# Kernel tuning notes

Measured on AMD Instinct MI355X. Metric: run time of the kernel, lower is better.

## Reference

```python
import jax, jax.numpy as jnp
import numpy as np

WINDOW_SIZE = 11
CHANNEL = 1
SIGMA = 1.5


def _gaussian_window(window_size=WINDOW_SIZE, channel=CHANNEL, sigma=SIGMA):
    x = np.arange(window_size)
    g = np.exp(-((x - window_size // 2) ** 2) / (2.0 * sigma ** 2))
    g = g / g.sum()
    w2d = np.outer(g, g).astype(np.float32)  # [K,K]
    # depthwise conv kernel: [C_out=channel, C_in/groups=1, K, K]
    return jnp.asarray(np.broadcast_to(w2d, (channel, 1, window_size, window_size)))


def _dwconv(x, window):
    pad = WINDOW_SIZE // 2
    return jax.lax.conv_general_dilated(
        x, window,
        window_strides=(1, 1),
        padding=[(pad, pad), (pad, pad)],
        dimension_numbers=('NCHW', 'OIHW', 'NCHW'),
        feature_group_count=CHANNEL)


def _ssim(img1, img2, window):
    C1 = 0.01 ** 2
    C2 = 0.03 ** 2
    mu1 = _dwconv(img1, window)
    mu2 = _dwconv(img2, window)
    mu1_sq = mu1 * mu1
    mu2_sq = mu2 * mu2
    mu1_mu2 = mu1 * mu2
    sigma1_sq = _dwconv(img1 * img1, window) - mu1_sq
    sigma2_sq = _dwconv(img2 * img2, window) - mu2_sq
    sigma12 = _dwconv(img1 * img2, window) - mu1_mu2
    ssim_map = ((2.0 * mu1_mu2 + C1) * (2.0 * sigma12 + C2)) / (
        (mu1_sq + mu2_sq + C1) * (sigma1_sq + sigma2_sq + C2))
    return ssim_map.mean()


def setup_inputs() -> dict:
    key = jax.random.key(0)
    k1, k2 = jax.random.split(key)
    B, C, H, W = 64, 1, 512, 512
    pred = jax.random.uniform(k1, (B, C, H, W), dtype=jnp.float32)
    target = jax.random.uniform(k2, (B, C, H, W), dtype=jnp.float32)
    return {"pred": pred, "target": target}


def reference(pred, target):
    window = _gaussian_window()
    return 1.0 - _ssim(pred[:, :1], target[:, :1], window)
```

## Files before the change

kernel.cpp:

```cpp
#include <hip/hip_runtime.h>

#define BATCH 64
#define HH 512
#define WW 512
#define TH 32
#define KS 11
#define PADK 5
#define NIN (TH + 2 * PADK)
#define LROW (WW + 2 * PADK)
#define NPIX (64.0 * 512.0 * 512.0)

__global__ void __launch_bounds__(512, 2) ssim_main_kernel(
    const float* __restrict__ img1, const float* __restrict__ img2,
    double* __restrict__ accum) {
  constexpr float GA[KS] = {
      0.00102838f, 0.00759884f, 0.03600087f, 0.10936069f, 0.21300553f,
      0.26601172f, 0.21300553f, 0.10936069f, 0.03600087f, 0.00759884f,
      0.00102838f};
  const float C1v = 1e-4f, C2v = 9e-4f;

  const int c  = threadIdx.x;
  const int r0 = blockIdx.x * TH;
  const int b  = blockIdx.y;

  const float* __restrict__ p1 = img1 + (size_t)b * (HH * WW);
  const float* __restrict__ p2 = img2 + (size_t)b * (HH * WW);

  __shared__ float4 s4[2][4][LROW];
  __shared__ float wsum[8];

  if (c < PADK) {
#pragma unroll
    for (int bi = 0; bi < 2; ++bi)
#pragma unroll
      for (int r = 0; r < 4; ++r) {
        s4[bi][r][c]             = make_float4(0.f, 0.f, 0.f, 0.f);
        s4[bi][r][WW + PADK + c] = make_float4(0.f, 0.f, 0.f, 0.f);
      }
  }

#define DECLR(s) float zA##s = 0.f, zB##s = 0.f, zQ##s = 0.f, zP##s = 0.f;
  DECLR(0) DECLR(1) DECLR(2) DECLR(3) DECLR(4) DECLR(5)
  DECLR(6) DECLR(7) DECLR(8) DECLR(9) DECLR(10)

  float pa0, pa1, pa2, pa3, pb0, pb1, pb2, pb3;
  float local = 0.f;

#define LD1(k_, j_)                                                     \
  {                                                                     \
    constexpr int rc_ = 4 * (k_) + (j_);                                \
    pa##j_ = 0.f; pb##j_ = 0.f;                                         \
    if constexpr (rc_ < NIN) {                                          \
      const int rr_ = r0 - PADK + rc_;                                  \
      if ((unsigned)rr_ < HH) {                                         \
        const int off_ = rr_ * WW + c;                                  \
        pa##j_ = p1[off_];                                              \
        pb##j_ = p2[off_];                                              \
      }                                                                 \
    }                                                                   \
  }
#define LOADC(k_) { LD1(k_, 0) LD1(k_, 1) LD1(k_, 2) LD1(k_, 3) }

#define WR1(k_, j_)                                                     \
  {                                                                     \
    constexpr int rc_ = 4 * (k_) + (j_);                                \
    if constexpr (rc_ < NIN)                                            \
      s4[(k_) & 1][j_][PADK + c] = make_float4(                         \
          pa##j_, pb##j_, fmaf(pa##j_, pa##j_, pb##j_ * pb##j_),        \
          pa##j_ * pb##j_);                                             \
  }
#define WRITEC(k_) { WR1(k_, 0) WR1(k_, 1) WR1(k_, 2) WR1(k_, 3) }

#define HBODY(bb_, j_, S)                                               \
  {                                                                     \
    float h1 = 0.f, h2 = 0.f, hq = 0.f, hp = 0.f;                       \
    _Pragma("unroll")                                                   \
    for (int k = 0; k < KS; ++k) {                                      \
      const float4 v = s4[bb_][j_][c + k];                              \
      const float w_ = GA[k];                                           \
      h1 = fmaf(w_, v.x, h1);                                           \
      h2 = fmaf(w_, v.y, h2);                                           \
      hq = fmaf(w_, v.z, hq);                                           \
      hp = fmaf(w_, v.w, hp);                                           \
    }                                                                   \
    zA##S = h1; zB##S = h2; zQ##S = hq; zP##S = hp;                     \
  }

#define VC(P, s0,s1,s2v,s3,s4v,s5,s6v,s7,s8,s9,s10)                     \
  fmaf(GA[10], P##s10, fmaf(GA[9], P##s9, fmaf(GA[8], P##s8,            \
  fmaf(GA[7], P##s7, fmaf(GA[6], P##s6v, fmaf(GA[5], P##s5,             \
  fmaf(GA[4], P##s4v, fmaf(GA[3], P##s3, fmaf(GA[2], P##s2v,            \
  fmaf(GA[1], P##s1, GA[0] * P##s0))))))))))

#define VOUTBODY(s0,s1,s2v,s3,s4v,s5,s6v,s7,s8,s9,s10)                  \
  {                                                                     \
    const float m1 = VC(zA, s0,s1,s2v,s3,s4v,s5,s6v,s7,s8,s9,s10);      \
    const float m2 = VC(zB, s0,s1,s2v,s3,s4v,s5,s6v,s7,s8,s9,s10);      \
    const float mq = VC(zQ, s0,s1,s2v,s3,s4v,s5,s6v,s7,s8,s9,s10);      \
    const float mp = VC(zP, s0,s1,s2v,s3,s4v,s5,s6v,s7,s8,s9,s10);      \
    const float m1s = m1 * m1, m2s = m2 * m2, m12 = m1 * m2;            \
    const float s12 = mp - m12;                                         \
    const float sqq = mq - m1s - m2s;                                   \
    const float num = fmaf(2.f, m12, C1v) * fmaf(2.f, s12, C2v);        \
    const float den = (m1s + m2s + C1v) * (sqq + C2v);                  \
    local = fmaf(num, __builtin_amdgcn_rcpf(den), local);               \
  }

#define ROT0  0,1,2,3,4,5,6,7,8,9,10
#define ROT1  1,2,3,4,5,6,7,8,9,10,0
#define ROT2  2,3,4,5,6,7,8,9,10,0,1
#define ROT3  3,4,5,6,7,8,9,10,0,1,2
#define ROT4  4,5,6,7,8,9,10,0,1,2,3
#define ROT5  5,6,7,8,9,10,0,1,2,3,4
#define ROT6  6,7,8,9,10,0,1,2,3,4,5
#define ROT7  7,8,9,10,0,1,2,3,4,5,6
#define ROT8  8,9,10,0,1,2,3,4,5,6,7
#define ROT9  9,10,0,1,2,3,4,5,6,7,8
#define ROT10 10,0,1,2,3,4,5,6,7,8,9
#define VOUTE(...) VOUTBODY(__VA_ARGS__)

#define ROWH(bb_, j_, S)      { HBODY(bb_, j_, S) }
#define ROWO(bb_, j_, S, R_)  { HBODY(bb_, j_, S) VOUTE(R_) }

  LOADC(0)

  WRITEC(0) __syncthreads(); LOADC(1)
  ROWH(0,0,0) ROWH(0,1,1) ROWH(0,2,2) ROWH(0,3,3)
  WRITEC(1) __syncthreads(); LOADC(2)
  ROWH(1,0,4) ROWH(1,1,5) ROWH(1,2,6) ROWH(1,3,7)
  WRITEC(2) __syncthreads(); LOADC(3)
  ROWH(0,0,8) ROWH(0,1,9)
  ROWO(0,2,10, ROT0) ROWO(0,3,0, ROT1)
  WRITEC(3) __syncthreads(); LOADC(4)
  ROWO(1,0,1, ROT2) ROWO(1,1,2, ROT3) ROWO(1,2,3, ROT4) ROWO(1,3,4, ROT5)
  WRITEC(4) __syncthreads(); LOADC(5)
  ROWO(0,0,5, ROT6) ROWO(0,1,6, ROT7) ROWO(0,2,7, ROT8) ROWO(0,3,8, ROT9)
  WRITEC(5) __syncthreads(); LOADC(6)
  ROWO(1,0,9, ROT10) ROWO(1,1,10, ROT0) ROWO(1,2,0, ROT1) ROWO(1,3,1, ROT2)
  WRITEC(6) __syncthreads(); LOADC(7)
  ROWO(0,0,2, ROT3) ROWO(0,1,3, ROT4) ROWO(0,2,4, ROT5) ROWO(0,3,5, ROT6)
  WRITEC(7) __syncthreads(); LOADC(8)
  ROWO(1,0,6, ROT7) ROWO(1,1,7, ROT8) ROWO(1,2,8, ROT9) ROWO(1,3,9, ROT10)
  WRITEC(8) __syncthreads(); LOADC(9)
  ROWO(0,0,10, ROT0) ROWO(0,1,0, ROT1) ROWO(0,2,1, ROT2) ROWO(0,3,2, ROT3)
  WRITEC(9) __syncthreads(); LOADC(10)
  ROWO(1,0,3, ROT4) ROWO(1,1,4, ROT5) ROWO(1,2,5, ROT6) ROWO(1,3,6, ROT7)
  WRITEC(10) __syncthreads();
  ROWO(0,0,7, ROT8) ROWO(0,1,8, ROT9)

#pragma unroll
  for (int off = 32; off > 0; off >>= 1) local += __shfl_down(local, off, 64);
  const int wave = threadIdx.x >> 6;
  const int lane = threadIdx.x & 63;
  if (lane == 0) wsum[wave] = local;
  __syncthreads();
  if (threadIdx.x == 0) {
    float s = 0.f;
#pragma unroll
    for (int w = 0; w < 8; ++w) s += wsum[w];
    atomicAdd(accum, (double)s);
  }
}

__global__ void ssim_final_kernel(const double* __restrict__ accum,
                                  float* __restrict__ out) {
  out[0] = 1.0f - (float)(accum[0] / NPIX);
}

extern "C" void kernel_launch(void* const* d_in, const int* in_sizes, int n_in,
                              void* d_out, int out_size, void* d_ws, size_t ws_size,
                              hipStream_t stream) {
  const float* img1 = (const float*)d_in[0];
  const float* img2 = (const float*)d_in[1];
  double* accum = (double*)d_ws;
  hipMemsetAsync(accum, 0, sizeof(double), stream);

  dim3 grid(HH / TH, BATCH);
  ssim_main_kernel<<<grid, 512, 0, stream>>>(img1, img2, accum);
  ssim_final_kernel<<<1, 1, 0, stream>>>(accum, (float*)d_out);
}
```

Measured before the change: 180.1 us.

## Store only image pairs in LDS and recompute products in horizontal pass

The shared-memory row buffer now holds float2 (img1, img2) pairs instead of float4 with precomputed squared and cross products, halving LDS footprint and write traffic. The horizontal pass reads aligned float4 chunks covering two pixels at a time, using per-thread parity-shifted weights (12 taps with a zero at one end) so odd and even columns share the same aligned reads. Six 16-byte LDS reads replace eleven per row. The cost is recomputing q and p per tap and extra FMAs on zero-weighted taps.

New measurement: 179.0 us. About the same (-0.6%).

```diff
diff --git a/kernel.cpp b/kernel.cpp
--- a/kernel.cpp
+++ b/kernel.cpp
@@ -7,7 +7,7 @@
 #define KS 11
 #define PADK 5
 #define NIN (TH + 2 * PADK)
-#define LROW (WW + 2 * PADK)
+#define NP2 524
 #define NPIX (64.0 * 512.0 * 512.0)
 
 __global__ void __launch_bounds__(512, 2) ssim_main_kernel(
@@ -26,18 +26,32 @@
   const float* __restrict__ p1 = img1 + (size_t)b * (HH * WW);
   const float* __restrict__ p2 = img2 + (size_t)b * (HH * WW);
 
-  __shared__ float4 s4[2][4][LROW];
+  __shared__ __align__(16) float2 s2[2][4][NP2];
   __shared__ float wsum[8];
 
-  if (c < PADK) {
+  if (c < 12) {
+    const int idx = (c < 6) ? c : (512 + c);
 #pragma unroll
     for (int bi = 0; bi < 2; ++bi)
 #pragma unroll
-      for (int r = 0; r < 4; ++r) {
-        s4[bi][r][c]             = make_float4(0.f, 0.f, 0.f, 0.f);
-        s4[bi][r][WW + PADK + c] = make_float4(0.f, 0.f, 0.f, 0.f);
-      }
-  }
+      for (int r = 0; r < 4; ++r) s2[bi][r][idx] = make_float2(0.f, 0.f);
+  }
+
+  const bool oddc = (c & 1);
+  const float w0  = oddc ? GA[0]  : 0.f;
+  const float w1  = oddc ? GA[1]  : GA[0];
+  const float w2  = oddc ? GA[2]  : GA[1];
+  const float w3  = oddc ? GA[3]  : GA[2];
+  const float w4  = oddc ? GA[4]  : GA[3];
+  const float w5  = oddc ? GA[5]  : GA[4];
+  const float w6  = oddc ? GA[6]  : GA[5];
+  const float w7  = oddc ? GA[7]  : GA[6];
+  const float w8  = oddc ? GA[8]  : GA[7];
+  const float w9  = oddc ? GA[9]  : GA[8];
+  const float w10 = oddc ? GA[10] : GA[9];
+  const float w11 = oddc ? 0.f    : GA[10];
+
+  const int pr0 = (c + 1) >> 1;
 
 #define DECLR(s) float zA##s = 0.f, zB##s = 0.f, zQ##s = 0.f, zP##s = 0.f;
   DECLR(0) DECLR(1) DECLR(2) DECLR(3) DECLR(4) DECLR(5)
@@ -65,24 +79,30 @@
   {                                                                     \
     constexpr int rc_ = 4 * (k_) + (j_);                                \
     if constexpr (rc_ < NIN)                                            \
-      s4[(k_) & 1][j_][PADK + c] = make_float4(                         \
-          pa##j_, pb##j_, fmaf(pa##j_, pa##j_, pb##j_ * pb##j_),        \
-          pa##j_ * pb##j_);                                             \
+      s2[(k_) & 1][j_][c + 6] = make_float2(pa##j_, pb##j_);            \
   }
 #define WRITEC(k_) { WR1(k_, 0) WR1(k_, 1) WR1(k_, 2) WR1(k_, 3) }
 
+#define HPX(aa_, bb2_, w_)                                              \
+  {                                                                     \
+    const float q_ = fmaf(aa_, aa_, bb2_ * bb2_);                       \
+    const float p_ = aa_ * bb2_;                                        \
+    h1 = fmaf(w_, aa_, h1); h2 = fmaf(w_, bb2_, h2);                    \
+    hq = fmaf(w_, q_, hq);  hp = fmaf(w_, p_, hp);                      \
+  }
+#define HPAIR(kk_, wA_, wB_)                                            \
+  {                                                                     \
+    const float4 v = r4_[pr0 + kk_];                                    \
+    HPX(v.x, v.y, wA_) HPX(v.z, v.w, wB_)                               \
+  }
+
 #define HBODY(bb_, j_, S)                                               \
   {                                                                     \
+    const float4* r4_ =                                                 \
+        reinterpret_cast<const float4*>(&s2[bb_][j_][0]);               \
     float h1 = 0.f, h2 = 0.f, hq = 0.f, hp = 0.f;                       \
-    _Pragma("unroll")                                                   \
-    for (int k = 0; k < KS; ++k) {                                      \
-      const float4 v = s4[bb_][j_][c + k];                              \
-      const float w_ = GA[k];                                           \
-      h1 = fmaf(w_, v.x, h1);                                           \
-      h2 = fmaf(w_, v.y, h2);                                           \
-      hq = fmaf(w_, v.z, hq);                                           \
-      hp = fmaf(w_, v.w, hp);                                           \
-    }                                                                   \
+    HPAIR(0, w0, w1)  HPAIR(1, w2, w3)  HPAIR(2, w4, w5)                \
+    HPAIR(3, w6, w7)  HPAIR(4, w8, w9)  HPAIR(5, w10, w11)              \
     zA##S = h1; zB##S = h2; zQ##S = hq; zP##S = hp;                     \
   }
 
```

## Process two adjacent columns per thread with float2 loads and shared window reuse

Applied to the files above, without the earlier changes.

Each thread now handles two neighbouring output columns. It loads float2 pairs from both images and stores raw pixel pairs in shared memory, so each LDS read feeds both horizontal convolutions. The squared and cross products are recomputed from the raw pairs during the horizontal pass instead of being stored. Block size halves to 256 threads and register state doubles (88 vertical accumulators), which raises register pressure and may cut occupancy or cause spills.

New measurement: 337.7 us. +87.6%, slower.

```diff
diff --git a/kernel.cpp b/kernel.cpp
--- a/kernel.cpp
+++ b/kernel.cpp
@@ -7,10 +7,10 @@
 #define KS 11
 #define PADK 5
 #define NIN (TH + 2 * PADK)
-#define LROW (WW + 2 * PADK)
+#define NF4 262
 #define NPIX (64.0 * 512.0 * 512.0)
 
-__global__ void __launch_bounds__(512, 2) ssim_main_kernel(
+__global__ void __launch_bounds__(256, 4) ssim_main_kernel(
     const float* __restrict__ img1, const float* __restrict__ img2,
     double* __restrict__ accum) {
   constexpr float GA[KS] = {
@@ -19,43 +19,44 @@
       0.00102838f};
   const float C1v = 1e-4f, C2v = 9e-4f;
 
-  const int c  = threadIdx.x;
+  const int t  = threadIdx.x;
   const int r0 = blockIdx.x * TH;
   const int b  = blockIdx.y;
 
-  const float* __restrict__ p1 = img1 + (size_t)b * (HH * WW);
-  const float* __restrict__ p2 = img2 + (size_t)b * (HH * WW);
-
-  __shared__ float4 s4[2][4][LROW];
-  __shared__ float wsum[8];
-
-  if (c < PADK) {
+  const float2* __restrict__ pp1 =
+      reinterpret_cast<const float2*>(img1 + (size_t)b * HH * WW);
+  const float2* __restrict__ pp2 =
+      reinterpret_cast<const float2*>(img2 + (size_t)b * HH * WW);
+
+  __shared__ float4 s4[2][4][NF4];
+  __shared__ float wsum[4];
+
+  if (t < 6) {
+    const int idx = (t < 3) ? t : (256 + t);
 #pragma unroll
     for (int bi = 0; bi < 2; ++bi)
 #pragma unroll
-      for (int r = 0; r < 4; ++r) {
-        s4[bi][r][c]             = make_float4(0.f, 0.f, 0.f, 0.f);
-        s4[bi][r][WW + PADK + c] = make_float4(0.f, 0.f, 0.f, 0.f);
-      }
-  }
-
-#define DECLR(s) float zA##s = 0.f, zB##s = 0.f, zQ##s = 0.f, zP##s = 0.f;
+      for (int r = 0; r < 4; ++r) s4[bi][r][idx] = make_float4(0.f, 0.f, 0.f, 0.f);
+  }
+
+#define DECLR(s) float xA##s = 0.f, xB##s = 0.f, xQ##s = 0.f, xP##s = 0.f, \
+                       yA##s = 0.f, yB##s = 0.f, yQ##s = 0.f, yP##s = 0.f;
   DECLR(0) DECLR(1) DECLR(2) DECLR(3) DECLR(4) DECLR(5)
   DECLR(6) DECLR(7) DECLR(8) DECLR(9) DECLR(10)
 
-  float pa0, pa1, pa2, pa3, pb0, pb1, pb2, pb3;
+  float2 ta0, ta1, ta2, ta3, tb0, tb1, tb2, tb3;
   float local = 0.f;
 
 #define LD1(k_, j_)                                                     \
   {                                                                     \
     constexpr int rc_ = 4 * (k_) + (j_);                                \
-    pa##j_ = 0.f; pb##j_ = 0.f;                                         \
+    ta##j_ = make_float2(0.f, 0.f); tb##j_ = make_float2(0.f, 0.f);     \
     if constexpr (rc_ < NIN) {                                          \
       const int rr_ = r0 - PADK + rc_;                                  \
       if ((unsigned)rr_ < HH) {                                         \
-        const int off_ = rr_ * WW + c;                                  \
-        pa##j_ = p1[off_];                                              \
-        pb##j_ = p2[off_];                                              \
+        const int off_ = rr_ * (WW / 2) + t;                            \
+        ta##j_ = pp1[off_];                                             \
+        tb##j_ = pp2[off_];                                             \
       }                                                                 \
     }                                                                   \
   }
@@ -65,25 +66,49 @@
   {                                                                     \
     constexpr int rc_ = 4 * (k_) + (j_);                                \
     if constexpr (rc_ < NIN)                                            \
-      s4[(k_) & 1][j_][PADK + c] = make_float4(                         \
-          pa##j_, pb##j_, fmaf(pa##j_, pa##j_, pb##j_ * pb##j_),        \
-          pa##j_ * pb##j_);                                             \
+      s4[(k_) & 1][j_][t + 3] =                                         \
+          make_float4(ta##j_.x, tb##j_.x, ta##j_.y, tb##j_.y);          \
   }
 #define WRITEC(k_) { WR1(k_, 0) WR1(k_, 1) WR1(k_, 2) WR1(k_, 3) }
 
-#define HBODY(bb_, j_, S)                                               \
-  {                                                                     \
-    float h1 = 0.f, h2 = 0.f, hq = 0.f, hp = 0.f;                       \
-    _Pragma("unroll")                                                   \
-    for (int k = 0; k < KS; ++k) {                                      \
-      const float4 v = s4[bb_][j_][c + k];                              \
-      const float w_ = GA[k];                                           \
-      h1 = fmaf(w_, v.x, h1);                                           \
-      h2 = fmaf(w_, v.y, h2);                                           \
-      hq = fmaf(w_, v.z, hq);                                           \
-      hp = fmaf(w_, v.w, hp);                                           \
-    }                                                                   \
-    zA##S = h1; zB##S = h2; zQ##S = hq; zP##S = hp;                     \
+#define HBODY(bb_, j_, S)                                                     \
+  {                                                                           \
+    float h0a = 0.f, h0b = 0.f, h0q = 0.f, h0p = 0.f;                         \
+    float h1a = 0.f, h1b = 0.f, h1q = 0.f, h1p = 0.f;                         \
+    _Pragma("unroll")                                                         \
+    for (int kk = 0; kk < 7; ++kk) {                                          \
+      const float4 v = s4[bb_][j_][t + kk];                                   \
+      if (kk >= 1) {                         \
+        const float qv_ = fmaf(v.x, v.x, v.y * v.y);                          \
+        const float pv_ = v.x * v.y;                                          \
+        if (kk <= 5) {                                                        \
+          const float w_ = GA[2 * kk - 1];                                    \
+          h0a = fmaf(w_, v.x, h0a); h0b = fmaf(w_, v.y, h0b);                 \
+          h0q = fmaf(w_, qv_, h0q); h0p = fmaf(w_, pv_, h0p);                 \
+        }                                                                     \
+        {                                                                     \
+          const float w_ = GA[2 * kk - 2];                                    \
+          h1a = fmaf(w_, v.x, h1a); h1b = fmaf(w_, v.y, h1b);                 \
+          h1q = fmaf(w_, qv_, h1q); h1p = fmaf(w_, pv_, h1p);                 \
+        }                                                                     \
+      }                                                                       \
+      if (kk <= 5) {                           \
+        const float qv_ = fmaf(v.z, v.z, v.w * v.w);                          \
+        const float pv_ = v.z * v.w;                                          \
+        {                                                                     \
+          const float w_ = GA[2 * kk];                                        \
+          h0a = fmaf(w_, v.z, h0a); h0b = fmaf(w_, v.w, h0b);                 \
+          h0q = fmaf(w_, qv_, h0q); h0p = fmaf(w_, pv_, h0p);                 \
+        }                                                                     \
+        if (kk >= 1) {                                                        \
+          const float w_ = GA[2 * kk - 1];                                    \
+          h1a = fmaf(w_, v.z, h1a); h1b = fmaf(w_, v.w, h1b);                 \
+          h1q = fmaf(w_, qv_, h1q); h1p = fmaf(w_, pv_, h1p);                 \
+        }                                                                     \
+      }                                                                       \
+    }                                                                         \
+    xA##S = h0a; xB##S = h0b; xQ##S = h0q; xP##S = h0p;                       \
+    yA##S = h1a; yB##S = h1b; yQ##S = h1q; yP##S = h1p;                       \
   }
 
 #define VC(P, s0,s1,s2v,s3,s4v,s5,s6v,s7,s8,s9,s10)                     \
@@ -92,18 +117,32 @@
   fmaf(GA[4], P##s4v, fmaf(GA[3], P##s3, fmaf(GA[2], P##s2v,            \
   fmaf(GA[1], P##s1, GA[0] * P##s0))))))))))
 
-#define VOUTBODY(s0,s1,s2v,s3,s4v,s5,s6v,s7,s8,s9,s10)                  \
-  {                                                                     \
-    const float m1 = VC(zA, s0,s1,s2v,s3,s4v,s5,s6v,s7,s8,s9,s10);      \
-    const float m2 = VC(zB, s0,s1,s2v,s3,s4v,s5,s6v,s7,s8,s9,s10);      \
-    const float mq = VC(zQ, s0,s1,s2v,s3,s4v,s5,s6v,s7,s8,s9,s10);      \
-    const float mp = VC(zP, s0,s1,s2v,s3,s4v,s5,s6v,s7,s8,s9,s10);      \
+#define SSIMACC                                                         \
+  {                                                                     \
     const float m1s = m1 * m1, m2s = m2 * m2, m12 = m1 * m2;            \
     const float s12 = mp - m12;                                         \
     const float sqq = mq - m1s - m2s;                                   \
     const float num = fmaf(2.f, m12, C1v) * fmaf(2.f, s12, C2v);        \
     const float den = (m1s + m2s + C1v) * (sqq + C2v);                  \
     local = fmaf(num, __builtin_amdgcn_rcpf(den), local);               \
+  }
+
+#define VOUTBODY(s0,s1,s2v,s3,s4v,s5,s6v,s7,s8,s9,s10)                  \
+  {                                                                     \
+    {                                                                   \
+      const float m1 = VC(xA, s0,s1,s2v,s3,s4v,s5,s6v,s7,s8,s9,s10);    \
+      const float m2 = VC(xB, s0,s1,s2v,s3,s4v,s5,s6v,s7,s8,s9,s10);    \
+      const float mq = VC(xQ, s0,s1,s2v,s3,s4v,s5,s6v,s7,s8,s9,s10);    \
+      const float mp = VC(xP, s0,s1,s2v,s3,s4v,s5,s6v,s7,s8,s9,s10);    \
+      SSIMACC                                                           \
+    }                                                                   \
+    {                                                                   \
+      const float m1 = VC(yA, s0,s1,s2v,s3,s4v,s5,s6v,s7,s8,s9,s10);    \
+      const float m2 = VC(yB, s0,s1,s2v,s3,s4v,s5,s6v,s7,s8,s9,s10);    \
+      const float mq = VC(yQ, s0,s1,s2v,s3,s4v,s5,s6v,s7,s8,s9,s10);    \
+      const float mp = VC(yP, s0,s1,s2v,s3,s4v,s5,s6v,s7,s8,s9,s10);    \
+      SSIMACC                                                           \
+    }                                                                   \
   }
 
 #define ROT0  0,1,2,3,4,5,6,7,8,9,10
@@ -150,14 +189,12 @@
 
 #pragma unroll
   for (int off = 32; off > 0; off >>= 1) local += __shfl_down(local, off, 64);
-  const int wave = threadIdx.x >> 6;
-  const int lane = threadIdx.x & 63;
+  const int wave = t >> 6;
+  const int lane = t & 63;
   if (lane == 0) wsum[wave] = local;
   __syncthreads();
-  if (threadIdx.x == 0) {
-    float s = 0.f;
-#pragma unroll
-    for (int w = 0; w < 8; ++w) s += wsum[w];
+  if (t == 0) {
+    float s = wsum[0] + wsum[1] + wsum[2] + wsum[3];
     atomicAdd(accum, (double)s);
   }
 }
@@ -176,6 +213,6 @@
   hipMemsetAsync(accum, 0, sizeof(double), stream);
 
   dim3 grid(HH / TH, BATCH);
-  ssim_main_kernel<<<grid, 512, 0, stream>>>(img1, img2, accum);
+  ssim_main_kernel<<<grid, 256, 0, stream>>>(img1, img2, accum);
   ssim_final_kernel<<<1, 1, 0, stream>>>(accum, (float*)d_out);
 }
```

## Pack two pixels per float4 in LDS and load rows as float2

Applied to the files above, without the earlier changes.

Changes the shared-memory layout so each float4 holds two adjacent pixels of both images, with products computed on the fly, and each thread loads float2 from global memory. Thread halves handle even/odd output columns using wave-uniform weight selection via readfirstlane, so six float4 LDS reads replace eleven per row. This aims to cut LDS traffic and global load instruction count. In exchange it recomputes the squares and cross products inside the horizontal pass, and the new thread-to-row mapping is subtle.

Result: no change. 183.3 us (+1.8%).

```diff
diff --git a/kernel.cpp b/kernel.cpp
--- a/kernel.cpp
+++ b/kernel.cpp
@@ -7,7 +7,7 @@
 #define KS 11
 #define PADK 5
 #define NIN (TH + 2 * PADK)
-#define LROW (WW + 2 * PADK)
+#define NF4 262
 #define NPIX (64.0 * 512.0 * 512.0)
 
 __global__ void __launch_bounds__(512, 2) ssim_main_kernel(
@@ -19,72 +19,87 @@
       0.00102838f};
   const float C1v = 1e-4f, C2v = 9e-4f;
 
-  const int c  = threadIdx.x;
+  const int t  = threadIdx.x;
   const int r0 = blockIdx.x * TH;
   const int b  = blockIdx.y;
 
-  const float* __restrict__ p1 = img1 + (size_t)b * (HH * WW);
-  const float* __restrict__ p2 = img2 + (size_t)b * (HH * WW);
+  const float2* __restrict__ pp1 =
+      reinterpret_cast<const float2*>(img1 + (size_t)b * HH * WW);
+  const float2* __restrict__ pp2 =
+      reinterpret_cast<const float2*>(img2 + (size_t)b * HH * WW);
 
-  __shared__ float4 s4[2][4][LROW];
+  __shared__ float4 s4[2][4][NF4];
   __shared__ float wsum[8];
 
-  if (c < PADK) {
+  if (t < 6) {
+    const int idx = (t < 3) ? t : (256 + t);
 #pragma unroll
     for (int bi = 0; bi < 2; ++bi)
 #pragma unroll
-      for (int r = 0; r < 4; ++r) {
-        s4[bi][r][c]             = make_float4(0.f, 0.f, 0.f, 0.f);
-        s4[bi][r][WW + PADK + c] = make_float4(0.f, 0.f, 0.f, 0.f);
-      }
+      for (int r = 0; r < 4; ++r) s4[bi][r][idx] = make_float4(0.f, 0.f, 0.f, 0.f);
   }
+
+  const int pi = t & 255;
+  const int jA = (t >> 8) & 1;
+  const int jB = jA + 2;
+  const int base = pi + jA;
+
+#define RFL(x) __int_as_float(__builtin_amdgcn_readfirstlane(__float_as_int(x)))
+  const bool oddp = ((__builtin_amdgcn_readfirstlane(t) >> 8) & 1) != 0;
+  const float wx0 = RFL(oddp ? GA[0]  : 0.f);
+  const float wx1 = RFL(oddp ? GA[2]  : GA[1]);
+  const float wx2 = RFL(oddp ? GA[4]  : GA[3]);
+  const float wx3 = RFL(oddp ? GA[6]  : GA[5]);
+  const float wx4 = RFL(oddp ? GA[8]  : GA[7]);
+  const float wx5 = RFL(oddp ? GA[10] : GA[9]);
+  const float wz0 = RFL(oddp ? GA[1]  : GA[0]);
+  const float wz1 = RFL(oddp ? GA[3]  : GA[2]);
+  const float wz2 = RFL(oddp ? GA[5]  : GA[4]);
+  const float wz3 = RFL(oddp ? GA[7]  : GA[6]);
+  const float wz4 = RFL(oddp ? GA[9]  : GA[8]);
+  const float wz5 = RFL(oddp ? 0.f    : GA[10]);
 
 #define DECLR(s) float zA##s = 0.f, zB##s = 0.f, zQ##s = 0.f, zP##s = 0.f;
   DECLR(0) DECLR(1) DECLR(2) DECLR(3) DECLR(4) DECLR(5)
   DECLR(6) DECLR(7) DECLR(8) DECLR(9) DECLR(10)
 
-  float pa0, pa1, pa2, pa3, pb0, pb1, pb2, pb3;
+  float2 taA, tbA, taB, tbB;
   float local = 0.f;
 
-#define LD1(k_, j_)                                                     \
-  {                                                                     \
-    constexpr int rc_ = 4 * (k_) + (j_);                                \
-    pa##j_ = 0.f; pb##j_ = 0.f;                                         \
-    if constexpr (rc_ < NIN) {                                          \
-      const int rr_ = r0 - PADK + rc_;                                  \
-      if ((unsigned)rr_ < HH) {                                         \
-        const int off_ = rr_ * WW + c;                                  \
-        pa##j_ = p1[off_];                                              \
-        pb##j_ = p2[off_];                                              \
-      }                                                                 \
-    }                                                                   \
-  }
-#define LOADC(k_) { LD1(k_, 0) LD1(k_, 1) LD1(k_, 2) LD1(k_, 3) }
+#define LOADC(k_) {                                                     \
+    taA = make_float2(0.f, 0.f); tbA = make_float2(0.f, 0.f);           \
+    taB = make_float2(0.f, 0.f); tbB = make_float2(0.f, 0.f);           \
+    { const int rr_ = r0 - PADK + 4 * (k_) + jA;                        \
+      if ((unsigned)rr_ < HH) { const int o_ = rr_ * (WW / 2) + pi;     \
+        taA = pp1[o_]; tbA = pp2[o_]; } }                               \
+    if (4 * (k_) + jB < NIN) {                                          \
+      const int rr_ = r0 - PADK + 4 * (k_) + jB;                        \
+      if ((unsigned)rr_ < HH) { const int o_ = rr_ * (WW / 2) + pi;     \
+        taB = pp1[o_]; tbB = pp2[o_]; } } }
 
-#define WR1(k_, j_)                                                     \
-  {                                                                     \
-    constexpr int rc_ = 4 * (k_) + (j_);                                \
-    if constexpr (rc_ < NIN)                                            \
-      s4[(k_) & 1][j_][PADK + c] = make_float4(                         \
-          pa##j_, pb##j_, fmaf(pa##j_, pa##j_, pb##j_ * pb##j_),        \
-          pa##j_ * pb##j_);                                             \
-  }
-#define WRITEC(k_) { WR1(k_, 0) WR1(k_, 1) WR1(k_, 2) WR1(k_, 3) }
+#define WRITEC(k_) {                                                    \
+    s4[(k_) & 1][jA][pi + 3] = make_float4(taA.x, tbA.x, taA.y, tbA.y); \
+    if (4 * (k_) + jB < NIN)                                            \
+      s4[(k_) & 1][jB][pi + 3] =                                        \
+          make_float4(taB.x, tbB.x, taB.y, tbB.y); }
 
-#define HBODY(bb_, j_, S)                                               \
-  {                                                                     \
+#define HK(bb_, j_, kk_, wx_, wz_) {                                    \
+    const float4 v = s4[bb_][j_][base + kk_];                           \
+    const float qx_ = fmaf(v.x, v.x, v.y * v.y);                        \
+    const float px_ = v.x * v.y;                                        \
+    h1 = fmaf(wx_, v.x, h1); h2 = fmaf(wx_, v.y, h2);                   \
+    hq = fmaf(wx_, qx_, hq); hp = fmaf(wx_, px_, hp);                   \
+    const float qz_ = fmaf(v.z, v.z, v.w * v.w);                        \
+    const float pz_ = v.z * v.w;                                        \
+    h1 = fmaf(wz_, v.z, h1); h2 = fmaf(wz_, v.w, h2);                   \
+    hq = fmaf(wz_, qz_, hq); hp = fmaf(wz_, pz_, hp); }
+
+#define HBODY(bb_, j_, S) {                                             \
     float h1 = 0.f, h2 = 0.f, hq = 0.f, hp = 0.f;                       \
-    _Pragma("unroll")                                                   \
-    for (int k = 0; k < KS; ++k) {                                      \
-      const float4 v = s4[bb_][j_][c + k];                              \
-      const float w_ = GA[k];                                           \
-      h1 = fmaf(w_, v.x, h1);                                           \
-      h2 = fmaf(w_, v.y, h2);                                           \
-      hq = fmaf(w_, v.z, hq);                                           \
-      hp = fmaf(w_, v.w, hp);                                           \
-    }                                                                   \
-    zA##S = h1; zB##S = h2; zQ##S = hq; zP##S = hp;                     \
-  }
+    HK(bb_, j_, 0, wx0, wz0) HK(bb_, j_, 1, wx1, wz1)                   \
+    HK(bb_, j_, 2, wx2, wz2) HK(bb_, j_, 3, wx3, wz3)                   \
+    HK(bb_, j_, 4, wx4, wz4) HK(bb_, j_, 5, wx5, wz5)                   \
+    zA##S = h1; zB##S = h2; zQ##S = hq; zP##S = hp; }
 
 #define VC(P, s0,s1,s2v,s3,s4v,s5,s6v,s7,s8,s9,s10)                     \
   fmaf(GA[10], P##s10, fmaf(GA[9], P##s9, fmaf(GA[8], P##s8,            \
@@ -150,11 +165,11 @@
 
 #pragma unroll
   for (int off = 32; off > 0; off >>= 1) local += __shfl_down(local, off, 64);
-  const int wave = threadIdx.x >> 6;
-  const int lane = threadIdx.x & 63;
+  const int wave = t >> 6;
+  const int lane = t & 63;
   if (lane == 0) wsum[wave] = local;
   __syncthreads();
-  if (threadIdx.x == 0) {
+  if (t == 0) {
     float s = 0.f;
 #pragma unroll
     for (int w = 0; w < 8; ++w) s += wsum[w];
```
